# Optimization experiments

Hardware: AMD Instinct MI355X
Metric: run time of the kernel (lower is better)

## Reference

```python
import jax, jax.numpy as jnp
import numpy as np

B, T, D, H, L, F, V = 2, 512, 512, 8, 6, 2048, 32000
EPS = 1e-6


def _ln(x, g, b):
    m = x.mean(-1, keepdims=True)
    v = ((x - m) ** 2).mean(-1, keepdims=True)
    return (x - m) / jnp.sqrt(v + EPS) * g + b


def _mha(qx, kx, qkv_w, qkv_b, ow, ob, mask):
    # Wide heads: each head has dim D (Linear(D, H*D) projections, Linear(H*D, D) output).
    Bq, Tq, _ = qx.shape
    def proj(xx, w, bi):
        return (xx @ w + bi).reshape(Bq, Tq, H, D).transpose(0, 2, 1, 3)  # (B,H,T,D)
    q = proj(qx, qkv_w[0], qkv_b[0])
    k = proj(kx, qkv_w[1], qkv_b[1])
    v = proj(kx, qkv_w[2], qkv_b[2])
    s = jnp.einsum('bhqd,bhkd->bhqk', q, k) / jnp.sqrt(jnp.float32(D))
    if mask is not None:
        s = jnp.where(mask, s, -jnp.inf)
    w = jax.nn.softmax(s, axis=-1)
    o = jnp.einsum('bhqk,bhkd->bhqd', w, v).transpose(0, 2, 1, 3).reshape(Bq, Tq, H * D)
    return o @ ow + ob


def _pe(t, d):
    pos = jnp.arange(t, dtype=jnp.float32)[:, None]
    wl = jnp.exp(jnp.arange(0, d, 2, dtype=jnp.float32) / d * -jnp.log(10000.0))
    pe = jnp.zeros((t, d), dtype=jnp.float32)
    pe = pe.at[:, 0::2].set(jnp.sin(pos * wl))
    pe = pe.at[:, 1::2].set(jnp.cos(pos * wl))
    return pe


def _forward(x, y, enc_emb, dec_emb, enc_qkv_w, enc_qkv_b, enc_out_w, enc_out_b,
             enc_ln1_g, enc_ln1_b, enc_ff_w1, enc_ff_b1, enc_ff_w2, enc_ff_b2,
             enc_ln2_g, enc_ln2_b, dec_sa_qkv_w, dec_sa_qkv_b, dec_sa_out_w, dec_sa_out_b,
             dec_ln1_g, dec_ln1_b, dec_ca_qkv_w, dec_ca_qkv_b, dec_ca_out_w, dec_ca_out_b,
             dec_ln2_g, dec_ln2_b, dec_ff_w1, dec_ff_b1, dec_ff_w2, dec_ff_b2,
             dec_ln3_g, dec_ln3_b, head_w, head_b):
    pe = _pe(T, D)
    scale = jnp.sqrt(jnp.float32(D))
    # ---- encoder ----
    h = enc_emb[x] * scale + pe  # (B,T,D)
    for i in range(L):
        a = _mha(h, h, enc_qkv_w[i], enc_qkv_b[i], enc_out_w[i], enc_out_b[i], None)
        h = _ln(a + h, enc_ln1_g[i], enc_ln1_b[i])
        f = jax.nn.relu(h @ enc_ff_w1[i] + enc_ff_b1[i]) @ enc_ff_w2[i] + enc_ff_b2[i]
        h = _ln(f + h, enc_ln2_g[i], enc_ln2_b[i])
    # ---- decoder ----
    causal = jnp.tril(jnp.ones((T, T), dtype=bool))[None, None]  # (1,1,T,T)
    d = dec_emb[y] * scale + pe
    for i in range(L):
        a = _mha(d, d, dec_sa_qkv_w[i], dec_sa_qkv_b[i], dec_sa_out_w[i], dec_sa_out_b[i], causal)
        d = _ln(a + d, dec_ln1_g[i], dec_ln1_b[i])
        c = _mha(d, h, dec_ca_qkv_w[i], dec_ca_qkv_b[i], dec_ca_out_w[i], dec_ca_out_b[i], None)
        d = _ln(c + d, dec_ln2_g[i], dec_ln2_b[i])
        f = jax.nn.relu(d @ dec_ff_w1[i] + dec_ff_b1[i]) @ dec_ff_w2[i] + dec_ff_b2[i]
        d = _ln(f + d, dec_ln3_g[i], dec_ln3_b[i])
    return d @ head_w + head_b  # (B,T,V) logits


def setup_inputs() -> dict:
    key = jax.random.key(0)
    ks = iter(jax.random.split(key, 40))
    def nrm(shape):
        return jax.random.normal(next(ks), shape, dtype=jnp.float32) * 0.02
    HD = H * D
    return {
        'x': jax.random.randint(next(ks), (B, T), 0, V, dtype=jnp.int32),
        'y': jax.random.randint(next(ks), (B, T), 0, V, dtype=jnp.int32),
        'enc_emb': nrm((V, D)), 'dec_emb': nrm((V, D)),
        'enc_qkv_w': nrm((L, 3, D, HD)), 'enc_qkv_b': jnp.zeros((L, 3, HD)),
        'enc_out_w': nrm((L, HD, D)), 'enc_out_b': jnp.zeros((L, D)),
        'enc_ln1_g': jnp.ones((L, D)), 'enc_ln1_b': jnp.zeros((L, D)),
        'enc_ff_w1': nrm((L, D, F)), 'enc_ff_b1': jnp.zeros((L, F)),
        'enc_ff_w2': nrm((L, F, D)), 'enc_ff_b2': jnp.zeros((L, D)),
        'enc_ln2_g': jnp.ones((L, D)), 'enc_ln2_b': jnp.zeros((L, D)),
        'dec_sa_qkv_w': nrm((L, 3, D, HD)), 'dec_sa_qkv_b': jnp.zeros((L, 3, HD)),
        'dec_sa_out_w': nrm((L, HD, D)), 'dec_sa_out_b': jnp.zeros((L, D)),
        'dec_ln1_g': jnp.ones((L, D)), 'dec_ln1_b': jnp.zeros((L, D)),
        'dec_ca_qkv_w': nrm((L, 3, D, HD)), 'dec_ca_qkv_b': jnp.zeros((L, 3, HD)),
        'dec_ca_out_w': nrm((L, HD, D)), 'dec_ca_out_b': jnp.zeros((L, D)),
        'dec_ln2_g': jnp.ones((L, D)), 'dec_ln2_b': jnp.zeros((L, D)),
        'dec_ff_w1': nrm((L, D, F)), 'dec_ff_b1': jnp.zeros((L, F)),
        'dec_ff_w2': nrm((L, F, D)), 'dec_ff_b2': jnp.zeros((L, D)),
        'dec_ln3_g': jnp.ones((L, D)), 'dec_ln3_b': jnp.zeros((L, D)),
        'head_w': nrm((D, V)), 'head_b': jnp.zeros((V,)),
    }


def reference(x, y, enc_emb, dec_emb, enc_qkv_w, enc_qkv_b, enc_out_w, enc_out_b,
              enc_ln1_g, enc_ln1_b, enc_ff_w1, enc_ff_b1, enc_ff_w2, enc_ff_b2,
              enc_ln2_g, enc_ln2_b, dec_sa_qkv_w, dec_sa_qkv_b, dec_sa_out_w, dec_sa_out_b,
              dec_ln1_g, dec_ln1_b, dec_ca_qkv_w, dec_ca_qkv_b, dec_ca_out_w, dec_ca_out_b,
              dec_ln2_g, dec_ln2_b, dec_ff_w1, dec_ff_b1, dec_ff_w2, dec_ff_b2,
              dec_ln3_g, dec_ln3_b, head_w, head_b):
    return _forward(x, y, enc_emb, dec_emb, enc_qkv_w, enc_qkv_b, enc_out_w, enc_out_b,
                    enc_ln1_g, enc_ln1_b, enc_ff_w1, enc_ff_b1, enc_ff_w2, enc_ff_b2,
                    enc_ln2_g, enc_ln2_b, dec_sa_qkv_w, dec_sa_qkv_b, dec_sa_out_w, dec_sa_out_b,
                    dec_ln1_g, dec_ln1_b, dec_ca_qkv_w, dec_ca_qkv_b, dec_ca_out_w, dec_ca_out_b,
                    dec_ln2_g, dec_ln2_b, dec_ff_w1, dec_ff_b1, dec_ff_w2, dec_ff_b2,
                    dec_ln3_g, dec_ln3_b, head_w, head_b)
```

## Files before the change

### kernel.cpp

```cpp
#include <hip/hip_runtime.h>
#include <hip/hip_bf16.h>

#define B_ 2
#define T_ 512
#define D_ 512
#define H_ 8
#define L_ 6
#define F_ 2048
#define V_ 32000
#define BT_ (B_ * T_)
#define HD_ (H_ * D_)
#define BH_ (B_ * H_)

typedef __attribute__((ext_vector_type(8))) short short8;
typedef __attribute__((ext_vector_type(4))) short short4v;
typedef __attribute__((ext_vector_type(4))) float f32x4;

__device__ __forceinline__ short f2b(float f) {
  __hip_bfloat16 h = __float2bfloat16(f);
  short u; __builtin_memcpy(&u, &h, 2); return u;
}
__device__ __forceinline__ void store_c(float* p, float v) { *p = v; }
__device__ __forceinline__ void store_c(short* p, float v) { *p = f2b(v); }

__global__ __launch_bounds__(256) void embed_kernel(
    const int* __restrict__ tok, const float* __restrict__ emb,
    float* __restrict__ out, short* __restrict__ out16)
{
  const int row = blockIdx.x;
  const int t = row & (T_ - 1);
  const int token = tok[row];
  const float* e = emb + (size_t)token * D_;
  float* o = out + (size_t)row * D_;
  short* o16 = out16 + (size_t)row * D_;
  const float scale = sqrtf((float)D_);
  const float nl = -logf(10000.0f);
  for (int d = threadIdx.x; d < D_; d += 256) {
    int i = d >> 1;
    float wl = expf(nl * (2.0f * (float)i) / (float)D_);
    float ang = (float)t * wl;
    float pe = (d & 1) ? cosf(ang) : sinf(ang);
    float v = e[d] * scale + pe;
    o[d] = v; o16[d] = f2b(v);
  }
}

template<bool BTM, typename OutT, int BM>
__global__ __launch_bounds__(256, 3) void mfma_gemm(
    const short* __restrict__ A, long lda, long a_hi, long a_lo, int a_once,
    const void* __restrict__ Bv, long ldb, long b_hi, long b_lo,
    OutT* __restrict__ C, long ldc, long c_hi, long c_lo, long pstride,
    short* __restrict__ Ct, int trans_hh, int relu, int cskip, int cklim,
    int K, int nh, int ksplit, float scale,
    const float* __restrict__ bias, long bias_stride)
{
  constexpr int SA = BM + 1;
  constexpr int AU = BM / 32;
  constexpr int WRN = (BM == 128) ? 2 : 1;
  constexpr int WN  = (BM == 128) ? 64 : 32;
  constexpr int NR  = WN / 16;
  __shared__ short8 As8[8 * SA];
  __shared__ short8 Bs8[8 * 129];
  const int tid = threadIdx.x;
  const int bh = blockIdx.z / ksplit;
  const int kz = blockIdx.z - bh * ksplit;
  const int bb = bh / nh, hh = bh - bb * nh;
  const long a_off = a_once ? (hh >= 1 ? a_lo : 0) : (long)hh * a_lo;
  const short* Ab = A + (long)bb * a_hi + a_off;
  const short* Bbs = (const short*)Bv + (long)bb * b_hi + (long)hh * b_lo;
  const float* Bbf = (const float*)Bv + (long)bb * b_hi + (long)hh * b_lo;
  OutT* Cb = C + (long)bb * c_hi + (long)hh * c_lo + (long)kz * pstride;

  const int gx = gridDim.x, gy = gridDim.y;
  const int nwg = gx * gy;
  int lin = blockIdx.y * gx + blockIdx.x;
  {
    const int xcd = lin & 7, idx = lin >> 3;
    const int q = nwg >> 3, r = nwg & 7;
    lin = (xcd < r ? xcd * (q + 1) : r * (q + 1) + (xcd - r) * q) + idx;
  }
  const int bn = (lin / gy) * 128;
  const int bm = (lin % gy) * BM;
  if (cskip && bn > bm + BM - 1) return;

  const int klen = K / ksplit, kbase = kz * klen;
  const int lane = tid & 63, wid = tid >> 6;
  const int wr = (WRN == 2) ? (wid >> 1) : 0;
  const int wc = (WRN == 2) ? (wid & 1) : wid;
  const int lg = lane >> 4, r16 = lane & 15;

  int arow[AU], acol[AU];
#pragma unroll
  for (int u = 0; u < AU; ++u) { int o = u * 256 + tid; arow[u] = o >> 3; acol[u] = o & 7; }
  int brow[4], bcol[4];
#pragma unroll
  for (int u = 0; u < 4; ++u) { int o = u * 256 + tid; brow[u] = o >> 3; bcol[u] = o & 7; }
  const int ncol = tid & 127, nsh = tid >> 7;

  short8 pa[AU];
  short8 pbt[4];
  float  pbn[4][8];

  auto load = [&](int k0) {
#pragma unroll
    for (int u = 0; u < AU; ++u)
      pa[u] = *(const short8*)(Ab + (long)(bm + arow[u]) * lda + (k0 + acol[u] * 8));
    if constexpr (BTM) {
#pragma unroll
      for (int u = 0; u < 4; ++u)
        pbt[u] = *(const short8*)(Bbs + (long)(bn + brow[u]) * ldb + (k0 + bcol[u] * 8));
    } else {
      const float* s = Bbf + (long)(k0 + nsh * 32) * ldb + (bn + ncol);
#pragma unroll
      for (int i = 0; i < 4; ++i)
#pragma unroll
        for (int j = 0; j < 8; ++j)
          pbn[i][j] = s[(long)(i * 8 + j) * ldb];
    }
  };
  auto stage = [&]() {
#pragma unroll
    for (int u = 0; u < AU; ++u) As8[acol[u] * SA + arow[u]] = pa[u];
    if constexpr (BTM) {
#pragma unroll
      for (int u = 0; u < 4; ++u) Bs8[bcol[u] * 129 + brow[u]] = pbt[u];
    } else {
#pragma unroll
      for (int i = 0; i < 4; ++i) {
        short8 v;
#pragma unroll
        for (int j = 0; j < 8; ++j) v[j] = f2b(pbn[i][j]);
        Bs8[(nsh * 4 + i) * 129 + ncol] = v;
      }
    }
  };

  f32x4 acc[4][NR] = {};
  auto domfma = [&]() {
#pragma unroll
    for (int kb = 0; kb < 2; ++kb) {
      const int cha = (kb * 4 + lg) * SA;
      const int chb = (kb * 4 + lg) * 129;
      short8 a0 = As8[cha + wr * 64 +  0 + r16];
      short8 a1 = As8[cha + wr * 64 + 16 + r16];
      short8 a2 = As8[cha + wr * 64 + 32 + r16];
      short8 a3 = As8[cha + wr * 64 + 48 + r16];
#pragma unroll
      for (int n = 0; n < NR; ++n) {
        short8 bfr = Bs8[chb + wc * WN + n * 16 + r16];
        acc[0][n] = __builtin_amdgcn_mfma_f32_16x16x32_bf16(a0, bfr, acc[0][n], 0, 0, 0);
        acc[1][n] = __builtin_amdgcn_mfma_f32_16x16x32_bf16(a1, bfr, acc[1][n], 0, 0, 0);
        acc[2][n] = __builtin_amdgcn_mfma_f32_16x16x32_bf16(a2, bfr, acc[2][n], 0, 0, 0);
        acc[3][n] = __builtin_amdgcn_mfma_f32_16x16x32_bf16(a3, bfr, acc[3][n], 0, 0, 0);
      }
    }
  };

  int nsteps = klen >> 6;
  if (cklim) { const int lim = (bm >> 6) + 1; if (lim < nsteps) nsteps = lim; }
  load(kbase);
  stage();
  __syncthreads();
  for (int t = 0; t < nsteps; ++t) {
    const bool more = (t + 1 < nsteps);
    if (more) load(kbase + (t + 1) * 64);
    domfma();
    if (more) { __syncthreads(); stage(); __syncthreads(); }
  }

  const float* bp = bias ? bias + (long)hh * bias_stride : nullptr;
  if (hh == trans_hh) {
#pragma unroll
    for (int m = 0; m < 4; ++m)
#pragma unroll
      for (int n = 0; n < NR; ++n) {
        const int col = bn + wc * WN + n * 16 + r16;
        const float badd = bp ? bp[col] : 0.0f;
        short4v sv;
#pragma unroll
        for (int rr = 0; rr < 4; ++rr) sv[rr] = f2b(acc[m][n][rr] * scale + badd);
        *(short4v*)(Ct + (long)col * BT_ + (bm + wr * 64 + m * 16 + lg * 4)) = sv;
      }
  } else {
#pragma unroll
    for (int m = 0; m < 4; ++m)
#pragma unroll
      for (int rr = 0; rr < 4; ++rr) {
        const int row = bm + wr * 64 + m * 16 + lg * 4 + rr;
        OutT* crow = Cb + (long)row * ldc + bn + wc * WN + r16;
#pragma unroll
        for (int n = 0; n < NR; ++n) {
          float v = acc[m][n][rr] * scale;
          if (bp) v += bp[bn + wc * WN + n * 16 + r16];
          if (relu) v = fmaxf(v, 0.0f);
          store_c(&crow[n * 16], v);
        }
      }
  }
}

__global__ __launch_bounds__(256) void reduce_ln_kernel(
    const float* __restrict__ P, long pstride, int ks,
    const float* __restrict__ bias, float* __restrict__ hbuf, short* __restrict__ h16,
    const float* __restrict__ gam, const float* __restrict__ bet)
{
  __shared__ float red[256];
  const int row = blockIdx.x, tid = threadIdx.x;
  const long base = (long)row * D_;
  float s0 = hbuf[base + tid] + bias[tid];
  float s1 = hbuf[base + tid + 256] + bias[tid + 256];
  for (int z = 0; z < ks; ++z) {
    s0 += P[(long)z * pstride + base + tid];
    s1 += P[(long)z * pstride + base + tid + 256];
  }
  red[tid] = s0 + s1; __syncthreads();
  for (int o = 128; o > 0; o >>= 1) { if (tid < o) red[tid] += red[tid + o]; __syncthreads(); }
  const float mean = red[0] * (1.0f / D_); __syncthreads();
  const float d0 = s0 - mean, d1 = s1 - mean;
  red[tid] = d0 * d0 + d1 * d1; __syncthreads();
  for (int o = 128; o > 0; o >>= 1) { if (tid < o) red[tid] += red[tid + o]; __syncthreads(); }
  const float inv = rsqrtf(red[0] * (1.0f / D_) + 1e-6f);
  const float v0 = d0 * inv * gam[tid] + bet[tid];
  const float v1 = d1 * inv * gam[tid + 256] + bet[tid + 256];
  hbuf[base + tid] = v0;       h16[base + tid] = f2b(v0);
  hbuf[base + tid + 256] = v1; h16[base + tid + 256] = f2b(v1);
}

__global__ __launch_bounds__(256) void softmax_kernel(
    const float* __restrict__ S, short* __restrict__ P, int causal)
{
  __shared__ float red[256];
  const int q = blockIdx.x, bh = blockIdx.y, tid = threadIdx.x;
  const float* row = S + ((size_t)bh * T_ + q) * T_;
  short* prow = P + ((size_t)bh * T_ + q) * T_;
  const int n = causal ? (q + 1) : T_;
  const float v0 = row[tid], v1 = row[tid + 256];
  const bool in0 = tid < n, in1 = (tid + 256) < n;
  red[tid] = fmaxf(in0 ? v0 : -3.0e38f, in1 ? v1 : -3.0e38f);
  __syncthreads();
  for (int o = 128; o > 0; o >>= 1) { if (tid < o) red[tid] = fmaxf(red[tid], red[tid + o]); __syncthreads(); }
  const float m = red[0]; __syncthreads();
  const float e0 = in0 ? expf(v0 - m) : 0.0f;
  const float e1 = in1 ? expf(v1 - m) : 0.0f;
  red[tid] = e0 + e1; __syncthreads();
  for (int o = 128; o > 0; o >>= 1) { if (tid < o) red[tid] += red[tid + o]; __syncthreads(); }
  const float inv = 1.0f / red[0];
  prow[tid] = f2b(e0 * inv);
  prow[tid + 256] = f2b(e1 * inv);
}

extern "C" void kernel_launch(void* const* d_in, const int* in_sizes, int n_in,
                              void* d_out, int out_size, void* d_ws, size_t ws_size,
                              hipStream_t stream)
{
  const int*   x         = (const int*)d_in[0];
  const int*   y         = (const int*)d_in[1];
  const float* enc_emb   = (const float*)d_in[2];
  const float* dec_emb   = (const float*)d_in[3];
  const float* enc_qkv_w = (const float*)d_in[4];
  const float* enc_qkv_b = (const float*)d_in[5];
  const float* enc_out_w = (const float*)d_in[6];
  const float* enc_out_b = (const float*)d_in[7];
  const float* enc_ln1_g = (const float*)d_in[8];
  const float* enc_ln1_b = (const float*)d_in[9];
  const float* enc_ff_w1 = (const float*)d_in[10];
  const float* enc_ff_b1 = (const float*)d_in[11];
  const float* enc_ff_w2 = (const float*)d_in[12];
  const float* enc_ff_b2 = (const float*)d_in[13];
  const float* enc_ln2_g = (const float*)d_in[14];
  const float* enc_ln2_b = (const float*)d_in[15];
  const float* dec_sa_qkv_w = (const float*)d_in[16];
  const float* dec_sa_qkv_b = (const float*)d_in[17];
  const float* dec_sa_out_w = (const float*)d_in[18];
  const float* dec_sa_out_b = (const float*)d_in[19];
  const float* dec_ln1_g = (const float*)d_in[20];
  const float* dec_ln1_b = (const float*)d_in[21];
  const float* dec_ca_qkv_w = (const float*)d_in[22];
  const float* dec_ca_qkv_b = (const float*)d_in[23];
  const float* dec_ca_out_w = (const float*)d_in[24];
  const float* dec_ca_out_b = (const float*)d_in[25];
  const float* dec_ln2_g = (const float*)d_in[26];
  const float* dec_ln2_b = (const float*)d_in[27];
  const float* dec_ff_w1 = (const float*)d_in[28];
  const float* dec_ff_b1 = (const float*)d_in[29];
  const float* dec_ff_w2 = (const float*)d_in[30];
  const float* dec_ff_b2 = (const float*)d_in[31];
  const float* dec_ln3_g = (const float*)d_in[32];
  const float* dec_ln3_b = (const float*)d_in[33];
  const float* head_w    = (const float*)d_in[34];
  const float* head_b    = (const float*)d_in[35];
  float* out = (float*)d_out;

  char* wsb = (char*)d_ws;
  size_t off = 0;
  auto carve = [&](size_t bytes) { char* p = wsb + off; off += (bytes + 255) & ~255ull; return p; };
  float* h    = (float*)carve((size_t)BT_ * D_ * 4);
  float* dd   = (float*)carve((size_t)BT_ * D_ * 4);
  short* hb16 = (short*)carve((size_t)BT_ * D_ * 2);
  short* db16 = (short*)carve((size_t)BT_ * D_ * 2);
  short* Qb   = (short*)carve((size_t)BT_ * HD_ * 2);
  short* Kb   = (short*)carve((size_t)BT_ * HD_ * 2);
  short* Vt   = (short*)carve((size_t)HD_ * BT_ * 2);
  float* Sb   = (float*)carve((size_t)BH_ * T_ * T_ * 4);
  short* Pb   = (short*)carve((size_t)BH_ * T_ * T_ * 2);
  short* Ob   = Qb;
  short* mid  = Qb;
  (void)ws_size;

  dim3 blk(256);
  const long TT  = (long)T_ * T_;
  const long THD = (long)T_ * HD_;
  const long WQKV = (long)D_ * HD_;

  auto gemm = [&](bool bt, bool of32, bool bm64, int relu, int cskip, int cklim,
                  const short* A, long lda, long a_hi, long a_lo, int a_once,
                  const void* Bp, long ldb, long b_hi, long b_lo,
                  void* Cp, long ldc, long c_hi, long c_lo, long pstride,
                  short* Ct, int trans_hh,
                  int M, int N, int K, int batch, int nh, int ksplit,
                  float scale, const float* bias, long bstride) {
    dim3 grd(N / 128, M / (bm64 ? 64 : 128), batch * ksplit);
    if (bm64) {
      if (bt) {
        if (of32) mfma_gemm<true , float, 64><<<grd, blk, 0, stream>>>(A, lda, a_hi, a_lo, a_once, Bp, ldb, b_hi, b_lo,
            (float*)Cp, ldc, c_hi, c_lo, pstride, Ct, trans_hh, relu, cskip, cklim, K, nh, ksplit, scale, bias, bstride);
        else      mfma_gemm<true , short, 64><<<grd, blk, 0, stream>>>(A, lda, a_hi, a_lo, a_once, Bp, ldb, b_hi, b_lo,
            (short*)Cp, ldc, c_hi, c_lo, pstride, Ct, trans_hh, relu, cskip, cklim, K, nh, ksplit, scale, bias, bstride);
      } else {
        if (of32) mfma_gemm<false, float, 64><<<grd, blk, 0, stream>>>(A, lda, a_hi, a_lo, a_once, Bp, ldb, b_hi, b_lo,
            (float*)Cp, ldc, c_hi, c_lo, pstride, Ct, trans_hh, relu, cskip, cklim, K, nh, ksplit, scale, bias, bstride);
        else      mfma_gemm<false, short, 64><<<grd, blk, 0, stream>>>(A, lda, a_hi, a_lo, a_once, Bp, ldb, b_hi, b_lo,
            (short*)Cp, ldc, c_hi, c_lo, pstride, Ct, trans_hh, relu, cskip, cklim, K, nh, ksplit, scale, bias, bstride);
      }
    } else {
      if (of32) mfma_gemm<false, float, 128><<<grd, blk, 0, stream>>>(A, lda, a_hi, a_lo, a_once, Bp, ldb, b_hi, b_lo,
          (float*)Cp, ldc, c_hi, c_lo, pstride, Ct, trans_hh, relu, cskip, cklim, K, nh, ksplit, scale, bias, bstride);
      else      mfma_gemm<false, short, 128><<<grd, blk, 0, stream>>>(A, lda, a_hi, a_lo, a_once, Bp, ldb, b_hi, b_lo,
          (short*)Cp, ldc, c_hi, c_lo, pstride, Ct, trans_hh, relu, cskip, cklim, K, nh, ksplit, scale, bias, bstride);
    }
  };

  auto attention = [&](const short* qsrc, const short* kvsrc, bool self,
                       const float* qkvw, const float* qkvb,
                       const float* ow, const float* ob,
                       float* resid, short* resid16, int causal,
                       const float* lng, const float* lnb) {
    gemm(false, false, true, 0, 0, 0, qsrc, D_, 0, (long)(kvsrc - qsrc), 1,
         qkvw, HD_, 0, WQKV,
         Qb, HD_, 0, (long)(Kb - Qb), 0, Vt, 2,
         BT_, HD_, D_, 3, 3, 1, 1.0f, qkvb, HD_);
    gemm(true, true, true, 0, causal, 0, Qb, HD_, THD, D_, 0, Kb, HD_, THD, D_,
         Sb, T_, (long)H_ * TT, TT, 0, nullptr, -1,
         T_, T_, D_, BH_, H_, 1, 0.044194173824159216f, nullptr, 0);
    softmax_kernel<<<dim3(T_, BH_), blk, 0, stream>>>(Sb, Pb, causal);
    gemm(true, false, true, 0, 0, causal, Pb, T_, (long)H_ * TT, TT, 0,
         Vt, BT_, T_, (long)D_ * BT_,
         Ob, HD_, THD, D_, 0, nullptr, -1,
         T_, D_, T_, BH_, H_, 1, 1.0f, nullptr, 0);
    gemm(false, true, true, 0, 0, 0, Ob, HD_, 0, 0, 0, ow, D_, 0, 0,
         Sb, D_, 0, 0, (long)BT_ * D_, nullptr, -1,
         BT_, D_, HD_, 1, 1, 8, 1.0f, nullptr, 0);
    reduce_ln_kernel<<<dim3(BT_), blk, 0, stream>>>(
        Sb, (long)BT_ * D_, 8, ob, resid, resid16, lng, lnb);
  };

  auto ffn = [&](float* resid, short* resid16,
                 const float* w1, const float* b1,
                 const float* w2, const float* b2,
                 const float* lng, const float* lnb) {
    gemm(false, false, true, 1, 0, 0, resid16, D_, 0, 0, 0, w1, F_, 0, 0,
         mid, F_, 0, 0, 0, nullptr, -1,
         BT_, F_, D_, 1, 1, 1, 1.0f, b1, 0);
    gemm(false, true, true, 0, 0, 0, mid, F_, 0, 0, 0, w2, D_, 0, 0,
         Sb, D_, 0, 0, (long)BT_ * D_, nullptr, -1,
         BT_, D_, F_, 1, 1, 8, 1.0f, nullptr, 0);
    reduce_ln_kernel<<<dim3(BT_), blk, 0, stream>>>(
        Sb, (long)BT_ * D_, 8, b2, resid, resid16, lng, lnb);
  };

  embed_kernel<<<dim3(BT_), blk, 0, stream>>>(x, enc_emb, h, hb16);
  for (int i = 0; i < L_; ++i) {
    attention(hb16, hb16, true,
              enc_qkv_w + (size_t)i * 3 * WQKV, enc_qkv_b + (size_t)i * 3 * HD_,
              enc_out_w + (size_t)i * HD_ * D_, enc_out_b + (size_t)i * D_,
              h, hb16, 0, enc_ln1_g + (size_t)i * D_, enc_ln1_b + (size_t)i * D_);
    ffn(h, hb16, enc_ff_w1 + (size_t)i * D_ * F_, enc_ff_b1 + (size_t)i * F_,
        enc_ff_w2 + (size_t)i * F_ * D_, enc_ff_b2 + (size_t)i * D_,
        enc_ln2_g + (size_t)i * D_, enc_ln2_b + (size_t)i * D_);
  }

  embed_kernel<<<dim3(BT_), blk, 0, stream>>>(y, dec_emb, dd, db16);
  for (int i = 0; i < L_; ++i) {
    attention(db16, db16, true,
              dec_sa_qkv_w + (size_t)i * 3 * WQKV, dec_sa_qkv_b + (size_t)i * 3 * HD_,
              dec_sa_out_w + (size_t)i * HD_ * D_, dec_sa_out_b + (size_t)i * D_,
              dd, db16, 1, dec_ln1_g + (size_t)i * D_, dec_ln1_b + (size_t)i * D_);
    attention(db16, hb16, false,
              dec_ca_qkv_w + (size_t)i * 3 * WQKV, dec_ca_qkv_b + (size_t)i * 3 * HD_,
              dec_ca_out_w + (size_t)i * HD_ * D_, dec_ca_out_b + (size_t)i * D_,
              dd, db16, 0, dec_ln2_g + (size_t)i * D_, dec_ln2_b + (size_t)i * D_);
    ffn(dd, db16, dec_ff_w1 + (size_t)i * D_ * F_, dec_ff_b1 + (size_t)i * F_,
        dec_ff_w2 + (size_t)i * F_ * D_, dec_ff_b2 + (size_t)i * D_,
        dec_ln3_g + (size_t)i * D_, dec_ln3_b + (size_t)i * D_);
  }

  gemm(false, true, false, 0, 0, 0, db16, D_, 0, 0, 0, head_w, V_, 0, 0,
       out, V_, 0, 0, 0, nullptr, -1,
       BT_, V_, D_, 1, 1, 1, 1.0f, head_b, 0);
}
```

Measured before the change: 2.350 ms.

## Pre-convert weights to transposed bf16 and use BT GEMM path; reduce split-K to 4

Adds a transpose-and-convert kernel that turns every fp32 weight matrix into an N-major bf16 copy in workspace at the start of each call. All projection, FFN and head GEMMs then use the B-transposed bf16 kernel path instead of reading fp32 weights and converting them inside the GEMM. The split-K factor for the output and FFN2 GEMMs drops from 8 to 4, which shrinks the partial-sum buffer the reduce-LN kernel has to read. In exchange it needs extra workspace and a conversion pass over roughly 300M bytes of weights on every call.

```diff
diff --git a/kernel.cpp b/kernel.cpp
--- a/kernel.cpp
+++ b/kernel.cpp
@@ -43,6 +43,25 @@
     float v = e[d] * scale + pe;
     o[d] = v; o16[d] = f2b(v);
   }
+}
+
+__global__ __launch_bounds__(256) void wconv_kernel(
+    const float* __restrict__ in, short* __restrict__ outp, int K, int N)
+{
+  __shared__ float tile[64][65];
+  const long mstride = (long)K * N;
+  const float* src = in + (long)blockIdx.z * mstride;
+  short* dst = outp + (long)blockIdx.z * mstride;
+  const int k0 = blockIdx.y * 64, n0 = blockIdx.x * 64;
+  const int tid = threadIdx.x;
+  const int r = tid >> 6, c = tid & 63;
+#pragma unroll
+  for (int i = 0; i < 16; ++i)
+    tile[r + i * 4][c] = src[(long)(k0 + r + i * 4) * N + n0 + c];
+  __syncthreads();
+#pragma unroll
+  for (int i = 0; i < 16; ++i)
+    dst[(long)(n0 + r + i * 4) * K + k0 + c] = f2b(tile[c][r + i * 4]);
 }
 
 template<bool BTM, typename OutT, int BM>
@@ -305,12 +324,42 @@
   short* Pb   = (short*)carve((size_t)BH_ * T_ * T_ * 2);
   short* Ob   = Qb;
   short* mid  = Qb;
-  (void)ws_size;
+
+  const size_t QKVG = (size_t)L_ * 3 * D_ * HD_;
+  const size_t OUTG = (size_t)L_ * HD_ * D_;
+  const size_t FFG  = (size_t)L_ * D_ * F_;
+  const size_t HEADG = (size_t)D_ * V_;
+  const size_t conv_bytes = (3 * QKVG + 3 * OUTG + 2 * FFG + 2 * FFG + HEADG) * 2 + 4096;
+  const bool WBT = (ws_size >= off + conv_bytes);
+  short *Weq = nullptr, *Wdsq = nullptr, *Wdcq = nullptr;
+  short *Weo = nullptr, *Wdso = nullptr, *Wdco = nullptr;
+  short *Wef1 = nullptr, *Wef2 = nullptr, *Wdf1 = nullptr, *Wdf2 = nullptr, *Whd = nullptr;
+  if (WBT) {
+    Weq  = (short*)carve(QKVG * 2);  Wdsq = (short*)carve(QKVG * 2);  Wdcq = (short*)carve(QKVG * 2);
+    Weo  = (short*)carve(OUTG * 2);  Wdso = (short*)carve(OUTG * 2);  Wdco = (short*)carve(OUTG * 2);
+    Wef1 = (short*)carve(FFG * 2);   Wef2 = (short*)carve(FFG * 2);
+    Wdf1 = (short*)carve(FFG * 2);   Wdf2 = (short*)carve(FFG * 2);
+    Whd  = (short*)carve(HEADG * 2);
+  }
 
   dim3 blk(256);
   const long TT  = (long)T_ * T_;
   const long THD = (long)T_ * HD_;
   const long WQKV = (long)D_ * HD_;
+
+  if (WBT) {
+    wconv_kernel<<<dim3(HD_/64, D_/64, 3 * L_), blk, 0, stream>>>(enc_qkv_w, Weq, D_, HD_);
+    wconv_kernel<<<dim3(HD_/64, D_/64, 3 * L_), blk, 0, stream>>>(dec_sa_qkv_w, Wdsq, D_, HD_);
+    wconv_kernel<<<dim3(HD_/64, D_/64, 3 * L_), blk, 0, stream>>>(dec_ca_qkv_w, Wdcq, D_, HD_);
+    wconv_kernel<<<dim3(D_/64, HD_/64, L_), blk, 0, stream>>>(enc_out_w, Weo, HD_, D_);
+    wconv_kernel<<<dim3(D_/64, HD_/64, L_), blk, 0, stream>>>(dec_sa_out_w, Wdso, HD_, D_);
+    wconv_kernel<<<dim3(D_/64, HD_/64, L_), blk, 0, stream>>>(dec_ca_out_w, Wdco, HD_, D_);
+    wconv_kernel<<<dim3(F_/64, D_/64, L_), blk, 0, stream>>>(enc_ff_w1, Wef1, D_, F_);
+    wconv_kernel<<<dim3(D_/64, F_/64, L_), blk, 0, stream>>>(enc_ff_w2, Wef2, F_, D_);
+    wconv_kernel<<<dim3(F_/64, D_/64, L_), blk, 0, stream>>>(dec_ff_w1, Wdf1, D_, F_);
+    wconv_kernel<<<dim3(D_/64, F_/64, L_), blk, 0, stream>>>(dec_ff_w2, Wdf2, F_, D_);
+    wconv_kernel<<<dim3(V_/64, D_/64, 1), blk, 0, stream>>>(head_w, Whd, D_, V_);
+  }
 
   auto gemm = [&](bool bt, bool of32, bool bm64, int relu, int cskip, int cklim,
                   const short* A, long lda, long a_hi, long a_lo, int a_once,
@@ -333,22 +382,37 @@
             (short*)Cp, ldc, c_hi, c_lo, pstride, Ct, trans_hh, relu, cskip, cklim, K, nh, ksplit, scale, bias, bstride);
       }
     } else {
-      if (of32) mfma_gemm<false, float, 128><<<grd, blk, 0, stream>>>(A, lda, a_hi, a_lo, a_once, Bp, ldb, b_hi, b_lo,
-          (float*)Cp, ldc, c_hi, c_lo, pstride, Ct, trans_hh, relu, cskip, cklim, K, nh, ksplit, scale, bias, bstride);
-      else      mfma_gemm<false, short, 128><<<grd, blk, 0, stream>>>(A, lda, a_hi, a_lo, a_once, Bp, ldb, b_hi, b_lo,
-          (short*)Cp, ldc, c_hi, c_lo, pstride, Ct, trans_hh, relu, cskip, cklim, K, nh, ksplit, scale, bias, bstride);
+      if (bt) {
+        if (of32) mfma_gemm<true , float, 128><<<grd, blk, 0, stream>>>(A, lda, a_hi, a_lo, a_once, Bp, ldb, b_hi, b_lo,
+            (float*)Cp, ldc, c_hi, c_lo, pstride, Ct, trans_hh, relu, cskip, cklim, K, nh, ksplit, scale, bias, bstride);
+        else      mfma_gemm<true , short, 128><<<grd, blk, 0, stream>>>(A, lda, a_hi, a_lo, a_once, Bp, ldb, b_hi, b_lo,
+            (short*)Cp, ldc, c_hi, c_lo, pstride, Ct, trans_hh, relu, cskip, cklim, K, nh, ksplit, scale, bias, bstride);
+      } else {
+        if (of32) mfma_gemm<false, float, 128><<<grd, blk, 0, stream>>>(A, lda, a_hi, a_lo, a_once, Bp, ldb, b_hi, b_lo,
+            (float*)Cp, ldc, c_hi, c_lo, pstride, Ct, trans_hh, relu, cskip, cklim, K, nh, ksplit, scale, bias, bstride);
+        else      mfma_gemm<false, short, 128><<<grd, blk, 0, stream>>>(A, lda, a_hi, a_lo, a_once, Bp, ldb, b_hi, b_lo,
+            (short*)Cp, ldc, c_hi, c_lo, pstride, Ct, trans_hh, relu, cskip, cklim, K, nh, ksplit, scale, bias, bstride);
+      }
     }
   };
 
-  auto attention = [&](const short* qsrc, const short* kvsrc, bool self,
-                       const float* qkvw, const float* qkvb,
-                       const float* ow, const float* ob,
+  const int KS = 4;
+
+  auto attention = [&](const short* qsrc, const short* kvsrc,
+                       const float* qkvw, const short* qkvw16, const float* qkvb,
+                       const float* ow, const short* ow16, const float* ob,
                        float* resid, short* resid16, int causal,
                        const float* lng, const float* lnb) {
-    gemm(false, false, true, 0, 0, 0, qsrc, D_, 0, (long)(kvsrc - qsrc), 1,
-         qkvw, HD_, 0, WQKV,
-         Qb, HD_, 0, (long)(Kb - Qb), 0, Vt, 2,
-         BT_, HD_, D_, 3, 3, 1, 1.0f, qkvb, HD_);
+    if (WBT)
+      gemm(true, false, true, 0, 0, 0, qsrc, D_, 0, (long)(kvsrc - qsrc), 1,
+           qkvw16, D_, 0, WQKV,
+           Qb, HD_, 0, (long)(Kb - Qb), 0, Vt, 2,
+           BT_, HD_, D_, 3, 3, 1, 1.0f, qkvb, HD_);
+    else
+      gemm(false, false, true, 0, 0, 0, qsrc, D_, 0, (long)(kvsrc - qsrc), 1,
+           qkvw, HD_, 0, WQKV,
+           Qb, HD_, 0, (long)(Kb - Qb), 0, Vt, 2,
+           BT_, HD_, D_, 3, 3, 1, 1.0f, qkvb, HD_);
     gemm(true, true, true, 0, causal, 0, Qb, HD_, THD, D_, 0, Kb, HD_, THD, D_,
          Sb, T_, (long)H_ * TT, TT, 0, nullptr, -1,
          T_, T_, D_, BH_, H_, 1, 0.044194173824159216f, nullptr, 0);
@@ -357,54 +421,86 @@
          Vt, BT_, T_, (long)D_ * BT_,
          Ob, HD_, THD, D_, 0, nullptr, -1,
          T_, D_, T_, BH_, H_, 1, 1.0f, nullptr, 0);
-    gemm(false, true, true, 0, 0, 0, Ob, HD_, 0, 0, 0, ow, D_, 0, 0,
-         Sb, D_, 0, 0, (long)BT_ * D_, nullptr, -1,
-         BT_, D_, HD_, 1, 1, 8, 1.0f, nullptr, 0);
+    if (WBT)
+      gemm(true, true, true, 0, 0, 0, Ob, HD_, 0, 0, 0, ow16, HD_, 0, 0,
+           Sb, D_, 0, 0, (long)BT_ * D_, nullptr, -1,
+           BT_, D_, HD_, 1, 1, KS, 1.0f, nullptr, 0);
+    else
+      gemm(false, true, true, 0, 0, 0, Ob, HD_, 0, 0, 0, ow, D_, 0, 0,
+           Sb, D_, 0, 0, (long)BT_ * D_, nullptr, -1,
+           BT_, D_, HD_, 1, 1, KS, 1.0f, nullptr, 0);
     reduce_ln_kernel<<<dim3(BT_), blk, 0, stream>>>(
-        Sb, (long)BT_ * D_, 8, ob, resid, resid16, lng, lnb);
+        Sb, (long)BT_ * D_, KS, ob, resid, resid16, lng, lnb);
   };
 
   auto ffn = [&](float* resid, short* resid16,
-                 const float* w1, const float* b1,
-                 const float* w2, const float* b2,
+                 const float* w1, const short* w116, const float* b1,
+                 const float* w2, const short* w216, const float* b2,
                  const float* lng, const float* lnb) {
-    gemm(false, false, true, 1, 0, 0, resid16, D_, 0, 0, 0, w1, F_, 0, 0,
-         mid, F_, 0, 0, 0, nullptr, -1,
-         BT_, F_, D_, 1, 1, 1, 1.0f, b1, 0);
-    gemm(false, true, true, 0, 0, 0, mid, F_, 0, 0, 0, w2, D_, 0, 0,
-         Sb, D_, 0, 0, (long)BT_ * D_, nullptr, -1,
-         BT_, D_, F_, 1, 1, 8, 1.0f, nullptr, 0);
+    if (WBT)
+      gemm(true, false, true, 1, 0, 0, resid16, D_, 0, 0, 0, w116, D_, 0, 0,
+           mid, F_, 0, 0, 0, nullptr, -1,
+           BT_, F_, D_, 1, 1, 1, 1.0f, b1, 0);
+    else
+      gemm(false, false, true, 1, 0, 0, resid16, D_, 0, 0, 0, w1, F_, 0, 0,
+           mid, F_, 0, 0, 0, nullptr, -1,
+           BT_, F_, D_, 1, 1, 1, 1.0f, b1, 0);
+    if (WBT)
+      gemm(true, true, true, 0, 0, 0, mid, F_, 0, 0, 0, w216, F_, 0, 0,
+           Sb, D_, 0, 0, (long)BT_ * D_, nullptr, -1,
+           BT_, D_, F_, 1, 1, KS, 1.0f, nullptr, 0);
+    else
+      gemm(false, true, true, 0, 0, 0, mid, F_, 0, 0, 0, w2, D_, 0, 0,
+           Sb, D_, 0, 0, (long)BT_ * D_, nullptr, -1,
+           BT_, D_, F_, 1, 1, KS, 1.0f, nullptr, 0);
     reduce_ln_kernel<<<dim3(BT_), blk, 0, stream>>>(
-        Sb, (long)BT_ * D_, 8, b2, resid, resid16, lng, lnb);
+        Sb, (long)BT_ * D_, KS, b2, resid, resid16, lng, lnb);
   };
 
   embed_kernel<<<dim3(BT_), blk, 0, stream>>>(x, enc_emb, h, hb16);
   for (int i = 0; i < L_; ++i) {
-    attention(hb16, hb16, true,
-              enc_qkv_w + (size_t)i * 3 * WQKV, enc_qkv_b + (size_t)i * 3 * HD_,
-              enc_out_w + (size_t)i * HD_ * D_, enc_out_b + (size_t)i * D_,
+    attention(hb16, hb16,
+              enc_qkv_w + (size_t)i * 3 * WQKV, WBT ? Weq + (size_t)i * 3 * WQKV : nullptr,
+              enc_qkv_b + (size_t)i * 3 * HD_,
+              enc_out_w + (size_t)i * HD_ * D_, WBT ? Weo + (size_t)i * HD_ * D_ : nullptr,
+              enc_out_b + (size_t)i * D_,
               h, hb16, 0, enc_ln1_g + (size_t)i * D_, enc_ln1_b + (size_t)i * D_);
-    ffn(h, hb16, enc_ff_w1 + (size_t)i * D_ * F_, enc_ff_b1 + (size_t)i * F_,
-        enc_ff_w2 + (size_t)i * F_ * D_, enc_ff_b2 + (size_t)i * D_,
+    ffn(h, hb16,
+        enc_ff_w1 + (size_t)i * D_ * F_, WBT ? Wef1 + (size_t)i * D_ * F_ : nullptr,
+        enc_ff_b1 + (size_t)i * F_,
+        enc_ff_w2 + (size_t)i * F_ * D_, WBT ? Wef2 + (size_t)i * F_ * D_ : nullptr,
+        enc_ff_b2 + (size_t)i * D_,
         enc_ln2_g + (size_t)i * D_, enc_ln2_b + (size_t)i * D_);
   }
 
   embed_kernel<<<dim3(BT_), blk, 0, stream>>>(y, dec_emb, dd, db16);
   for (int i = 0; i < L_; ++i) {
-    attention(db16, db16, true,
-              dec_sa_qkv_w + (size_t)i * 3 * WQKV, dec_sa_qkv_b + (size_t)i * 3 * HD_,
-              dec_sa_out_w + (size_t)i * HD_ * D_, dec_sa_out_b + (size_t)i * D_,
+    attention(db16, db16,
+              dec_sa_qkv_w + (size_t)i * 3 * WQKV, WBT ? Wdsq + (size_t)i * 3 * WQKV : nullptr,
+              dec_sa_qkv_b + (size_t)i * 3 * HD_,
+              dec_sa_out_w + (size_t)i * HD_ * D_, WBT ? Wdso + (size_t)i * HD_ * D_ : nullptr,
+              dec_sa_out_b + (size_t)i * D_,
               dd, db16, 1, dec_ln1_g + (size_t)i * D_, dec_ln1_b + (size_t)i * D_);
-    attention(db16, hb16, false,
-              dec_ca_qkv_w + (size_t)i * 3 * WQKV, dec_ca_qkv_b + (size_t)i * 3 * HD_,
-              dec_ca_out_w + (size_t)i * HD_ * D_, dec_ca_out_b + (size_t)i * D_,
+    attention(db16, hb16,
+              dec_ca_qkv_w + (size_t)i * 3 * WQKV, WBT ? Wdcq + (size_t)i * 3 * WQKV : nullptr,
+              dec_ca_qkv_b + (size_t)i * 3 * HD_,
+              dec_ca_out_w + (size_t)i * HD_ * D_, WBT ? Wdco + (size_t)i * HD_ * D_ : nullptr,
+              dec_ca_out_b + (size_t)i * D_,
               dd, db16, 0, dec_ln2_g + (size_t)i * D_, dec_ln2_b + (size_t)i * D_);
-    ffn(dd, db16, dec_ff_w1 + (size_t)i * D_ * F_, dec_ff_b1 + (size_t)i * F_,
-        dec_ff_w2 + (size_t)i * F_ * D_, dec_ff_b2 + (size_t)i * D_,
+    ffn(dd, db16,
+        dec_ff_w1 + (size_t)i * D_ * F_, WBT ? Wdf1 + (size_t)i * D_ * F_ : nullptr,
+        dec_ff_b1 + (size_t)i * F_,
+        dec_ff_w2 + (size_t)i * F_ * D_, WBT ? Wdf2 + (size_t)i * F_ * D_ : nullptr,
+        dec_ff_b2 + (size_t)i * D_,
         dec_ln3_g + (size_t)i * D_, dec_ln3_b + (size_t)i * D_);
   }
 
-  gemm(false, true, false, 0, 0, 0, db16, D_, 0, 0, 0, head_w, V_, 0, 0,
-       out, V_, 0, 0, 0, nullptr, -1,
-       BT_, V_, D_, 1, 1, 1, 1.0f, head_b, 0);
-}
+  if (WBT)
+    gemm(true, true, false, 0, 0, 0, db16, D_, 0, 0, 0, Whd, D_, 0, 0,
+         out, V_, 0, 0, 0, nullptr, -1,
+         BT_, V_, D_, 1, 1, 1, 1.0f, head_b, 0);
+  else
+    gemm(false, true, false, 0, 0, 0, db16, D_, 0, 0, 0, head_w, V_, 0, 0,
+         out, V_, 0, 0, 0, nullptr, -1,
+         BT_, V_, D_, 1, 1, 1, 1.0f, head_b, 0);
+}
```

Result: no change. 2.343 ms (-0.3%).
